# Performance work log

Measured on AMD Instinct MI355X. Metric: run time of the kernel, lower is better.

## Reference

```python
import jax, jax.numpy as jnp
import numpy as np

EPS = 1e-08


def _norm(H, add):
    # Faithful to GTN.norm: transpose, mask/set diagonal, row-normalize by degree, transpose back.
    # The original O(N^3) mm(deg_inv_diag, H) is expressed as an O(N^2) row scaling (same math).
    Ht = H.T
    n = Ht.shape[0]
    eye = jnp.eye(n, dtype=H.dtype)
    Ht = Ht * (1.0 - eye)
    if add:
        Ht = Ht + eye
    deg = jnp.sum(Ht, axis=1)
    deg_inv = jnp.where(deg == 0, 0.0, 1.0 / (deg + EPS))
    return (deg_inv[:, None] * Ht).T


def _gtconv(A, w):
    # A: [E, N, N]; w: [C, E, 1, 1] -> softmax over E, weighted sum of adjacency channels.
    s = jax.nn.softmax(w[:, :, 0, 0], axis=1)  # [C, E]
    return jnp.einsum('ce,eij->cij', s, A)     # [C, N, N]


def setup_inputs() -> dict:
    key = jax.random.key(0)
    k = jax.random.split(key, 6)
    E, N, C, w_in, w_out = 5, 2048, 2, 256, 64
    A = jax.random.uniform(k[0], (E, N, N), dtype=jnp.float32)
    X = jax.random.normal(k[1], (N, w_in), dtype=jnp.float32)
    conv_w_l0_1 = jax.random.normal(k[2], (C, E, 1, 1), dtype=jnp.float32)
    conv_w_l0_2 = jax.random.normal(k[3], (C, E, 1, 1), dtype=jnp.float32)
    conv_w_l1 = jax.random.normal(k[4], (C, E, 1, 1), dtype=jnp.float32)
    gcn_weight = jax.random.normal(k[5], (w_in, w_out), dtype=jnp.float32) * (1.0 / np.sqrt(w_in))
    return {"A": A, "X": X, "conv_w_l0_1": conv_w_l0_1, "conv_w_l0_2": conv_w_l0_2,
            "conv_w_l1": conv_w_l1, "gcn_weight": gcn_weight}


def reference(A, X, conv_w_l0_1, conv_w_l0_2, conv_w_l1, gcn_weight):
    N = A.shape[1]
    # Layer 0 (first=True): two GTConvs, meta-path composition via bmm.
    a = _gtconv(A, conv_w_l0_1)            # [C, N, N]
    b = _gtconv(A, conv_w_l0_2)            # [C, N, N]
    H = jnp.einsum('cij,cjk->cik', a, b)   # [C, N, N]
    # Layer 1 (first=False): normalize per channel, then compose with new conv.
    H = jax.vmap(lambda h: _norm(h, False))(H)
    a1 = _gtconv(A, conv_w_l1)
    H = jnp.einsum('cij,cjk->cik', H, a1)
    # GCN readout per channel: mm(norm_add(H_c).T, X @ W), relu, concat along features.
    Xw = X @ gcn_weight                     # [N, w_out]
    Hn = jax.vmap(lambda h: _norm(h, True))(H)   # [C, N, N]
    Xc = jax.nn.relu(jnp.einsum('cji,jk->cik', Hn, Xw))  # [C, N, w_out]
    X_ = jnp.transpose(Xc, (1, 0, 2)).reshape(N, -1)     # [N, C*w_out]
    return X_
```

## Files before the change

### kernel.cpp

```cpp
#include <hip/hip_runtime.h>
#include <cstdint>
#include <cstddef>

typedef unsigned short u16;
typedef __attribute__((ext_vector_type(8))) short short8;
typedef __attribute__((ext_vector_type(4))) float v4f;

static constexpr size_t NN = (size_t)2048 * 2048;
#define N2 2048

typedef __attribute__((address_space(1))) const unsigned int guint;
typedef __attribute__((address_space(3))) unsigned int luint;

__device__ __forceinline__ float b2f_bits(uint32_t hi) { union { uint32_t u; float f; } v; v.u = hi; return v.f; }
__device__ __forceinline__ float b2f(u16 x) { return b2f_bits((uint32_t)x << 16); }
__device__ __forceinline__ u16 f2b(float f) {
  union { float f; uint32_t u; } v; v.f = f;
  uint32_t r = v.u + 0x7fffu + ((v.u >> 16) & 1u);
  return (u16)(r >> 16);
}
__device__ __forceinline__ uint4 pack8(const float* f) {
  uint4 u;
  u.x = (uint32_t)f2b(f[0]) | ((uint32_t)f2b(f[1]) << 16);
  u.y = (uint32_t)f2b(f[2]) | ((uint32_t)f2b(f[3]) << 16);
  u.z = (uint32_t)f2b(f[4]) | ((uint32_t)f2b(f[5]) << 16);
  u.w = (uint32_t)f2b(f[6]) | ((uint32_t)f2b(f[7]) << 16);
  return u;
}
__device__ __forceinline__ float sgprf(float x) {
  union { float f; int i; } v; v.f = x;
  v.i = __builtin_amdgcn_readfirstlane(v.i);
  return v.f;
}

__global__ __launch_bounds__(512, 2) void conv_kernel(
    const float* __restrict__ A, const float* __restrict__ w1,
    const float* __restrict__ w2, const float* __restrict__ w3,
    const float* __restrict__ X, const float* __restrict__ W,
    u16* __restrict__ abf, u16* __restrict__ bbt, u16* __restrict__ a1t,
    u16* __restrict__ a1r, u16* __restrict__ Xwt, int* __restrict__ counters)
{
  __shared__ u16 LT[2][64 * 64];
  const int t = threadIdx.x;
  const int i0 = blockIdx.y * 64, j0 = blockIdx.x * 64;
  const int m = t >> 3;
  const int cg = t & 7;
  const int n0 = cg * 8;

  if (blockIdx.x == 0 && blockIdx.y == 0 && t < 66) counters[t] = 0;

  float sc[3][2][5];
  {
    const float* wsrc[3] = { w1, w2, w3 };
    for (int q = 0; q < 3; ++q)
      for (int c = 0; c < 2; ++c) {
        float v[5], mx = -1e30f, sum = 0.f;
        #pragma unroll
        for (int e = 0; e < 5; ++e) { v[e] = wsrc[q][c * 5 + e]; mx = fmaxf(mx, v[e]); }
        #pragma unroll
        for (int e = 0; e < 5; ++e) { v[e] = expf(v[e] - mx); sum += v[e]; }
        #pragma unroll
        for (int e = 0; e < 5; ++e) sc[q][c][e] = sgprf(v[e] / sum);
      }
  }

  float av[2][8], bv[2][8], cv[2][8];
  #pragma unroll
  for (int c = 0; c < 2; ++c)
    #pragma unroll
    for (int u = 0; u < 8; ++u) { av[c][u] = 0.f; bv[c][u] = 0.f; cv[c][u] = 0.f; }

  #pragma unroll
  for (int e = 0; e < 5; ++e) {
    const float* base = A + (size_t)e * NN + (size_t)(i0 + m) * N2 + (j0 + n0);
    float4 x0 = ((const float4*)base)[0];
    float4 x1 = ((const float4*)base)[1];
    float f[8] = { x0.x, x0.y, x0.z, x0.w, x1.x, x1.y, x1.z, x1.w };
    #pragma unroll
    for (int c = 0; c < 2; ++c)
      #pragma unroll
      for (int u = 0; u < 8; ++u) {
        av[c][u] += sc[0][c][e] * f[u];
        bv[c][u] += sc[1][c][e] * f[u];
        cv[c][u] += sc[2][c][e] * f[u];
      }
  }

  #pragma unroll
  for (int c = 0; c < 2; ++c) {
    *(uint4*)(abf + (size_t)c * NN + (size_t)(i0 + m) * N2 + (j0 + n0)) = pack8(av[c]);
    *(uint4*)(a1r + (size_t)c * NN + (size_t)(i0 + m) * N2 + (j0 + n0)) = pack8(cv[c]);
  }
  const int swb = ((m >> 3) ^ cg) & 7;
  const int mlo = m & 7;
  const int on = t >> 3;
  const int mb = t & 7;
  const int src = on * 64 + (((mb ^ (on >> 3)) & 7) * 8);
  #pragma unroll
  for (int c = 0; c < 2; ++c) {
    if (c == 1) __syncthreads();
    #pragma unroll
    for (int u = 0; u < 8; ++u) {
      const int idx = (n0 + u) * 64 + swb * 8 + mlo;
      LT[0][idx] = f2b(bv[c][u]);
      LT[1][idx] = f2b(cv[c][u]);
    }
    __syncthreads();
    *(uint4*)(bbt + (size_t)c * NN + (size_t)(j0 + on) * N2 + (i0 + mb * 8)) =
        *(const uint4*)&LT[0][src];
    *(uint4*)(a1t + (size_t)c * NN + (size_t)(j0 + on) * N2 + (i0 + mb * 8)) =
        *(const uint4*)&LT[1][src];
  }
  if (blockIdx.y < 8) {
    const int n = (int)(blockIdx.y * 32 + blockIdx.x) * 8 + (t >> 6);
    const int k = t & 63;
    float acc = 0.f;
    for (int mm = 0; mm < 256; ++mm)
      acc += X[n * 256 + mm] * W[mm * 64 + k];
    Xwt[(size_t)k * N2 + n] = f2b(acc);
  }
}

__global__ __launch_bounds__(256, 3) void gemm_kernel(
    const u16* __restrict__ Ain, const u16* __restrict__ Btin,
    u16* __restrict__ Cout, float* __restrict__ csp, float* __restrict__ diag)
{
  const int c = blockIdx.z;
  const u16* Ac = Ain + (size_t)c * NN;
  const u16* Bc = Btin + (size_t)c * NN;
  const int m0 = blockIdx.y * 128, n0 = blockIdx.x * 128;
  const int t = threadIdx.x, w = t >> 6, lane = t & 63;
  const int quad = lane >> 4, r = lane & 15;
  __shared__ u16 SM[128 * 64 + 128 * 64];
  u16* As = SM;
  u16* Bs = SM + 128 * 64;

  v4f zero4 = { 0.f, 0.f, 0.f, 0.f };
  v4f acc[2][8];
  #pragma unroll
  for (int i = 0; i < 2; ++i)
    #pragma unroll
    for (int j = 0; j < 8; ++j) acc[i][j] = zero4;

  const int srow = lane >> 3;
  const int sgran = (lane & 7) ^ srow;

  for (int kt = 0; kt < 2048; kt += 64) {
    __syncthreads();
    #pragma unroll
    for (int i = 0; i < 4; ++i) {
      const int chunk = i * 4 + w;
      const u16* ga = Ac + (size_t)(m0 + chunk * 8 + srow) * N2 + kt + sgran * 8;
      __builtin_amdgcn_global_load_lds((guint*)ga, (luint*)(As + chunk * 512), 16, 0, 0);
    }
    #pragma unroll
    for (int i = 0; i < 4; ++i) {
      const int chunk = i * 4 + w;
      const u16* gb = Bc + (size_t)(n0 + chunk * 8 + srow) * N2 + kt + sgran * 8;
      __builtin_amdgcn_global_load_lds((guint*)gb, (luint*)(Bs + chunk * 512), 16, 0, 0);
    }
    __syncthreads();
    #pragma unroll
    for (int ks = 0; ks < 2; ++ks) {
      const int sl = ((ks * 4 + quad) ^ (r & 7)) * 8;
      short8 af[2], bf[8];
      #pragma unroll
      for (int i = 0; i < 2; ++i)
        af[i] = *(const short8*)(As + (w * 32 + i * 16 + r) * 64 + sl);
      #pragma unroll
      for (int j = 0; j < 8; ++j)
        bf[j] = *(const short8*)(Bs + (j * 16 + r) * 64 + sl);
      #pragma unroll
      for (int i = 0; i < 2; ++i)
        #pragma unroll
        for (int j = 0; j < 8; ++j)
          acc[i][j] = __builtin_amdgcn_mfma_f32_16x16x32_bf16(af[i], bf[j], acc[i][j], 0, 0, 0);
    }
  }
  if (blockIdx.x == blockIdx.y) {
    #pragma unroll
    for (int i = 0; i < 2; ++i) {
      const int rowg = m0 + w * 32 + i * 16 + quad * 4;
      #pragma unroll
      for (int j = 0; j < 8; ++j) {
        const int colg = n0 + j * 16 + r;
        #pragma unroll
        for (int g = 0; g < 4; ++g)
          if (rowg + g == colg) diag[c * N2 + colg] = acc[i][j][g];
      }
    }
  }
  float s[8];
  #pragma unroll
  for (int j = 0; j < 8; ++j) {
    s[j] = 0.f;
    #pragma unroll
    for (int i = 0; i < 2; ++i)
      #pragma unroll
      for (int g = 0; g < 4; ++g) s[j] += acc[i][j][g];
    s[j] += __shfl_xor(s[j], 16);
    s[j] += __shfl_xor(s[j], 32);
  }
  __syncthreads();
  float* csl = (float*)SM;
  if (quad == 0) {
    #pragma unroll
    for (int j = 0; j < 8; ++j) csl[w * 128 + j * 16 + r] = s[j];
  }
  __syncthreads();
  if (t < 128) {
    const float v = csl[t] + csl[128 + t] + csl[256 + t] + csl[384 + t];
    csp[((size_t)(c * 16) + blockIdx.y) * N2 + n0 + t] = v;
  }
  {
    u16* tb = SM;
    u16* Cc = Cout + (size_t)c * NN;
    #pragma unroll
    for (int h = 0; h < 2; ++h) {
      __syncthreads();
      #pragma unroll
      for (int i = 0; i < 2; ++i) {
        #pragma unroll
        for (int jl = 0; jl < 4; ++jl) {
          const int j = h * 4 + jl;
          #pragma unroll
          for (int g = 0; g < 4; ++g)
            tb[(jl * 16 + r) * 136 + (w * 32 + i * 16 + quad * 4 + g)] = f2b(acc[i][j][g]);
        }
      }
      __syncthreads();
      const int rown = t >> 2, seg = t & 3;
      const u16* ps = tb + rown * 136 + seg * 32;
      uint4* pd = (uint4*)(Cc + (size_t)(n0 + h * 64 + rown) * N2 + m0 + seg * 32);
      pd[0] = ((const uint4*)ps)[0];
      pd[1] = ((const uint4*)ps)[1];
      pd[2] = ((const uint4*)ps)[2];
      pd[3] = ((const uint4*)ps)[3];
    }
  }
}

__global__ __launch_bounds__(256) void zgemm_kernel(
    const u16* __restrict__ Ht, const u16* __restrict__ Xwt,
    const u16* __restrict__ a1r, const float* __restrict__ csp,
    const float* __restrict__ diag1, float* __restrict__ Zp,
    float* __restrict__ dp, float* __restrict__ cp,
    u16* __restrict__ Yt, float* __restrict__ diag2, float* __restrict__ dinv2,
    int* __restrict__ counters)
{
  const int c = blockIdx.z, split = blockIdx.y, mt = blockIdx.x;
  const int m0 = mt * 128;
  const u16* Ac = Ht + (size_t)c * NN;
  const int t = threadIdx.x, w = t >> 6, lane = t & 63;
  const int quad = lane >> 4, r = lane & 15;
  __shared__ u16 SMZ[128 * 64 + 64 * 64];
  u16* As = SMZ;
  u16* Bs = SMZ + 128 * 64;

  v4f zero4 = { 0.f, 0.f, 0.f, 0.f };
  v4f acc[2][4];
  #pragma unroll
  for (int i = 0; i < 2; ++i)
    #pragma unroll
    for (int j = 0; j < 4; ++j) acc[i][j] = zero4;

  const int srow = lane >> 3;
  const int sgran = (lane & 7) ^ srow;

  for (int kk = 0; kk < 4; ++kk) {
    const int kt = split * 256 + kk * 64;
    __syncthreads();
    #pragma unroll
    for (int i = 0; i < 4; ++i) {
      const int chunk = i * 4 + w;
      const u16* ga = Ac + (size_t)(m0 + chunk * 8 + srow) * N2 + kt + sgran * 8;
      __builtin_amdgcn_global_load_lds((guint*)ga, (luint*)(As + chunk * 512), 16, 0, 0);
    }
    #pragma unroll
    for (int i = 0; i < 2; ++i) {
      const int chunk = i * 4 + w;
      const u16* gb = Xwt + (size_t)(chunk * 8 + srow) * N2 + kt + sgran * 8;
      __builtin_amdgcn_global_load_lds((guint*)gb, (luint*)(Bs + chunk * 512), 16, 0, 0);
    }
    __syncthreads();
    #pragma unroll
    for (int ks = 0; ks < 2; ++ks) {
      const int sl = ((ks * 4 + quad) ^ (r & 7)) * 8;
      short8 af[2], bf[4];
      #pragma unroll
      for (int i = 0; i < 2; ++i)
        af[i] = *(const short8*)(As + (w * 32 + i * 16 + r) * 64 + sl);
      #pragma unroll
      for (int j = 0; j < 4; ++j)
        bf[j] = *(const short8*)(Bs + (j * 16 + r) * 64 + sl);
      #pragma unroll
      for (int i = 0; i < 2; ++i)
        #pragma unroll
        for (int j = 0; j < 4; ++j)
          acc[i][j] = __builtin_amdgcn_mfma_f32_16x16x32_bf16(af[i], bf[j], acc[i][j], 0, 0, 0);
    }
  }
  const size_t pbase = (size_t)(split * 2 + c) * 64;
  #pragma unroll
  for (int i = 0; i < 2; ++i) {
    const int rowg = m0 + w * 32 + i * 16 + quad * 4;
    #pragma unroll
    for (int j = 0; j < 4; ++j) {
      const int colg = j * 16 + r;
      *(v4f*)(Zp + (pbase + colg) * (size_t)N2 + rowg) = acc[i][j];
    }
  }
  __syncthreads();
  float* ci_l = (float*)SMZ;
  float* wv_l = ci_l + 128;
  if (t < 128) {
    const int i = m0 + t;
    float cs = 0.f;
    #pragma unroll
    for (int s = 0; s < 16; ++s) cs += csp[((size_t)(c * 16) + s) * N2 + i];
    const float deg = cs - diag1[c * N2 + i];
    const float v = (deg == 0.f) ? 0.f : 1.f / (deg + 1e-8f);
    ci_l[t] = v;
    wv_l[t] = v * deg;
  }
  __syncthreads();
  const int j4 = (t & 15) * 4, ig = t >> 4;
  float dacc[4][4], cacc[4][4];
  #pragma unroll
  for (int kk = 0; kk < 4; ++kk) {
    const int gj = split * 256 + kk * 64 + j4;
    #pragma unroll
    for (int u = 0; u < 4; ++u) { dacc[kk][u] = 0.f; cacc[kk][u] = 0.f; }
    for (int ii = 0; ii < 8; ++ii) {
      const int i = m0 + ig * 8 + ii;
      uint2 hu = *(const uint2*)(Ht  + (size_t)c * NN + (size_t)i * N2 + gj);
      uint2 au = *(const uint2*)(a1r + (size_t)c * NN + (size_t)i * N2 + gj);
      float h[4], a[4];
      h[0] = b2f_bits(hu.x << 16); h[1] = b2f_bits(hu.x & 0xffff0000u);
      h[2] = b2f_bits(hu.y << 16); h[3] = b2f_bits(hu.y & 0xffff0000u);
      a[0] = b2f_bits(au.x << 16); a[1] = b2f_bits(au.x & 0xffff0000u);
      a[2] = b2f_bits(au.y << 16); a[3] = b2f_bits(au.y & 0xffff0000u);
      const float cq = ci_l[ig * 8 + ii];
      const float wq = wv_l[ig * 8 + ii];
      #pragma unroll
      for (int u = 0; u < 4; ++u) {
        cacc[kk][u] += wq * a[u];
        const float tv = cq * h[u] * a[u];
        dacc[kk][u] += (i == gj + u) ? 0.f : tv;
      }
    }
  }
  float* red = ci_l + 256;
  __syncthreads();
  #pragma unroll
  for (int kk = 0; kk < 4; ++kk)
    #pragma unroll
    for (int u = 0; u < 4; ++u) red[ig * 256 + kk * 64 + j4 + u] = dacc[kk][u];
  __syncthreads();
  {
    float v = 0.f;
    #pragma unroll
    for (int g = 0; g < 16; ++g) v += red[g * 256 + t];
    dp[((size_t)(c * 16) + mt) * N2 + split * 256 + t] = v;
  }
  __syncthreads();
  #pragma unroll
  for (int kk = 0; kk < 4; ++kk)
    #pragma unroll
    for (int u = 0; u < 4; ++u) red[ig * 256 + kk * 64 + j4 + u] = cacc[kk][u];
  __syncthreads();
  {
    float v = 0.f;
    #pragma unroll
    for (int g = 0; g < 16; ++g) v += red[g * 256 + t];
    cp[((size_t)(c * 16) + mt) * N2 + split * 256 + t] = v;
  }
  __shared__ int yLast, fLast;
  __syncthreads();
  if (t == 0) {
    __threadfence();
    yLast = (atomicAdd(&counters[mt * 2 + c], 1) == 7);
    fLast = (atomicAdd(&counters[32 + c], 1) == 127);
  }
  __syncthreads();
  if (yLast) {
    __threadfence();
    const int i = m0 + (t & 127), kg = t >> 7;
    const float civ = ci_l[t & 127];
    const float d1 = diag1[c * N2 + i];
    for (int k2 = 0; k2 < 32; ++k2) {
      const int k = kg * 32 + k2;
      float z = 0.f;
      #pragma unroll
      for (int s = 0; s < 8; ++s)
        z += Zp[(size_t)((s * 2 + c) * 64 + k) * N2 + i];
      const float xw = b2f(Xwt[(size_t)k * N2 + i]);
      Yt[(size_t)(c * 64 + k) * N2 + i] = f2b(civ * (z - d1 * xw));
    }
  }
  if (fLast) {
    __threadfence();
    for (int q = t; q < 2048; q += 256) {
      float ds = 0.f, cs = 0.f;
      #pragma unroll
      for (int b = 0; b < 16; ++b) {
        ds += dp[((size_t)(c * 16) + b) * N2 + q];
        cs += cp[((size_t)(c * 16) + b) * N2 + q];
      }
      const float deg = cs - ds + 1.0f;
      diag2[c * N2 + q] = ds;
      dinv2[c * N2 + q] = (deg == 0.f) ? 0.f : 1.f / (deg + 1e-8f);
    }
  }
}

__global__ __launch_bounds__(256) void tgemm_kernel(
    const u16* __restrict__ a1t, const u16* __restrict__ Yt,
    float* __restrict__ Tp, const float* __restrict__ diag2,
    const float* __restrict__ dinv2, const u16* __restrict__ Xwt,
    float* __restrict__ out, int* __restrict__ counters)
{
  const int c = blockIdx.z, split = blockIdx.y, mt = blockIdx.x;
  const int m0 = mt * 128;
  const u16* Ac = a1t + (size_t)c * NN;
  const u16* Bc = Yt + (size_t)c * (64 * (size_t)N2);
  const int t = threadIdx.x, w = t >> 6, lane = t & 63;
  const int quad = lane >> 4, r = lane & 15;
  __shared__ u16 As[128 * 64];
  __shared__ u16 Bs[64 * 64];

  v4f zero4 = { 0.f, 0.f, 0.f, 0.f };
  v4f acc[2][4];
  #pragma unroll
  for (int i = 0; i < 2; ++i)
    #pragma unroll
    for (int j = 0; j < 4; ++j) acc[i][j] = zero4;

  const int srow = lane >> 3;
  const int sgran = (lane & 7) ^ srow;

  for (int kk = 0; kk < 4; ++kk) {
    const int kt = split * 256 + kk * 64;
    __syncthreads();
    #pragma unroll
    for (int i = 0; i < 4; ++i) {
      const int chunk = i * 4 + w;
      const u16* ga = Ac + (size_t)(m0 + chunk * 8 + srow) * N2 + kt + sgran * 8;
      __builtin_amdgcn_global_load_lds((guint*)ga, (luint*)(As + chunk * 512), 16, 0, 0);
    }
    #pragma unroll
    for (int i = 0; i < 2; ++i) {
      const int chunk = i * 4 + w;
      const u16* gb = Bc + (size_t)(chunk * 8 + srow) * N2 + kt + sgran * 8;
      __builtin_amdgcn_global_load_lds((guint*)gb, (luint*)(Bs + chunk * 512), 16, 0, 0);
    }
    __syncthreads();
    #pragma unroll
    for (int ks = 0; ks < 2; ++ks) {
      const int sl = ((ks * 4 + quad) ^ (r & 7)) * 8;
      short8 af[2], bf[4];
      #pragma unroll
      for (int i = 0; i < 2; ++i)
        af[i] = *(const short8*)(As + (w * 32 + i * 16 + r) * 64 + sl);
      #pragma unroll
      for (int j = 0; j < 4; ++j)
        bf[j] = *(const short8*)(Bs + (j * 16 + r) * 64 + sl);
      #pragma unroll
      for (int i = 0; i < 2; ++i)
        #pragma unroll
        for (int j = 0; j < 4; ++j)
          acc[i][j] = __builtin_amdgcn_mfma_f32_16x16x32_bf16(af[i], bf[j], acc[i][j], 0, 0, 0);
    }
  }
  const size_t pbase = (size_t)(split * 2 + c) * 2048;
  #pragma unroll
  for (int i = 0; i < 2; ++i) {
    const int rowg = m0 + w * 32 + i * 16 + quad * 4;
    #pragma unroll
    for (int j = 0; j < 4; ++j) {
      const int colg = j * 16 + r;
      #pragma unroll
      for (int g = 0; g < 4; ++g)
        Tp[(pbase + rowg + g) * 64 + colg] = acc[i][j][g];
    }
  }
  __shared__ int eLast;
  __syncthreads();
  if (t == 0) {
    __threadfence();
    eLast = (atomicAdd(&counters[34 + mt * 2 + c], 1) == 7);
  }
  __syncthreads();
  if (eLast) {
    __threadfence();
    const int k = t & 63, ig = t >> 6;
    for (int ii = 0; ii < 32; ++ii) {
      const int i = m0 + ig * 32 + ii;
      float T = 0.f;
      #pragma unroll
      for (int s = 0; s < 8; ++s)
        T += Tp[((size_t)(s * 2 + c) * 2048 + i) * 64 + k];
      const float hd = diag2[c * N2 + i];
      const float dv = dinv2[c * N2 + i];
      const float xw = b2f(Xwt[(size_t)k * N2 + i]);
      float v = dv * (T - hd * xw + xw);
      v = v > 0.f ? v : 0.f;
      out[(size_t)i * 128 + c * 64 + k] = v;
    }
  }
}

extern "C" void kernel_launch(void* const* d_in, const int* in_sizes, int n_in,
                              void* d_out, int out_size, void* d_ws, size_t ws_size,
                              hipStream_t stream) {
  const float* A  = (const float*)d_in[0];
  const float* X  = (const float*)d_in[1];
  const float* w1 = (const float*)d_in[2];
  const float* w2 = (const float*)d_in[3];
  const float* w3 = (const float*)d_in[4];
  const float* W  = (const float*)d_in[5];
  float* out = (float*)d_out;
  char* ws = (char*)d_ws;

  u16*   abf   = (u16*)(ws + 0);
  u16*   bbt   = (u16*)(ws + 16777216);
  u16*   a1t   = (u16*)(ws + 33554432);
  u16*   a1r   = (u16*)(ws + 50331648);
  u16*   Ht    = (u16*)(ws + 67108864);
  u16*   Xwt   = (u16*)(ws + 83886080);
  float* cspa  = (float*)(ws + 84148224);
  float* diag1 = (float*)(ws + 84410368);
  float* diag2 = (float*)(ws + 84426752);
  float* dinv2 = (float*)(ws + 84443136);
  int*   cnt   = (int*)  (ws + 84459520);
  float* Zp    = (float*)(ws + 0);
  float* dp    = (float*)(ws + 16777216);
  float* cp    = (float*)(ws + 17039360);
  u16*   Yt    = (u16*)(ws + 17301504);
  float* Tp    = (float*)(ws + 50331648);

  conv_kernel<<<dim3(32, 32), 512, 0, stream>>>(A, w1, w2, w3, X, W, abf, bbt, a1t, a1r, Xwt, cnt);
  gemm_kernel<<<dim3(16, 16, 2), 256, 0, stream>>>(abf, bbt, Ht, cspa, diag1);
  zgemm_kernel<<<dim3(16, 8, 2), 256, 0, stream>>>(Ht, Xwt, a1r, cspa, diag1, Zp, dp, cp, Yt, diag2, dinv2, cnt);
  tgemm_kernel<<<dim3(16, 8, 2), 256, 0, stream>>>(a1t, Yt, Tp, diag2, dinv2, Xwt, out, cnt);
}
```

Baseline: 258.6 us.

## Replace split-K partial buffers with atomic accumulation and fuse Y construction into tgemm

Both skinny GEMMs now accumulate their split-K results straight into zeroed Z and T buffers with float atomics, instead of writing per-split partials that a last-arriving block reduces. The Y = D^-1(Z - diag*Xw) operand is no longer materialized by zgemm's tail. Each tgemm block computes its 256-row slice of Y into LDS from Z, and the degree/diag2 reduction moves into tgemm's epilogue. Conv_kernel zeroes Z/T and spreads the Xw computation across all blocks. This removes serialized last-block tails and partial-buffer traffic, at the cost of atomic contention and redundant Y recomputation across the 16 m-tiles.

After: 262.3 us. No clear change (+1.4%).

```diff
diff --git a/kernel.cpp b/kernel.cpp
--- a/kernel.cpp
+++ b/kernel.cpp
@@ -38,16 +38,19 @@
     const float* __restrict__ w2, const float* __restrict__ w3,
     const float* __restrict__ X, const float* __restrict__ W,
     u16* __restrict__ abf, u16* __restrict__ bbt, u16* __restrict__ a1t,
-    u16* __restrict__ a1r, u16* __restrict__ Xwt, int* __restrict__ counters)
+    u16* __restrict__ a1r, u16* __restrict__ Xwt,
+    float* __restrict__ zeroZT, int* __restrict__ counters)
 {
   __shared__ u16 LT[2][64 * 64];
   const int t = threadIdx.x;
+  const int bid = (int)(blockIdx.y * 32 + blockIdx.x);
   const int i0 = blockIdx.y * 64, j0 = blockIdx.x * 64;
   const int m = t >> 3;
   const int cg = t & 7;
   const int n0 = cg * 8;
 
-  if (blockIdx.x == 0 && blockIdx.y == 0 && t < 66) counters[t] = 0;
+  zeroZT[(size_t)bid * 512 + t] = 0.f;
+  if (bid == 0 && t < 64) counters[t] = 0;
 
   float sc[3][2][5];
   {
@@ -111,8 +114,8 @@
     *(uint4*)(a1t + (size_t)c * NN + (size_t)(j0 + on) * N2 + (i0 + mb * 8)) =
         *(const uint4*)&LT[1][src];
   }
-  if (blockIdx.y < 8) {
-    const int n = (int)(blockIdx.y * 32 + blockIdx.x) * 8 + (t >> 6);
+  if (t < 128) {
+    const int n = bid * 2 + (t >> 6);
     const int k = t & 63;
     float acc = 0.f;
     for (int mm = 0; mm < 256; ++mm)
@@ -243,10 +246,8 @@
 __global__ __launch_bounds__(256) void zgemm_kernel(
     const u16* __restrict__ Ht, const u16* __restrict__ Xwt,
     const u16* __restrict__ a1r, const float* __restrict__ csp,
-    const float* __restrict__ diag1, float* __restrict__ Zp,
-    float* __restrict__ dp, float* __restrict__ cp,
-    u16* __restrict__ Yt, float* __restrict__ diag2, float* __restrict__ dinv2,
-    int* __restrict__ counters)
+    const float* __restrict__ diag1, float* __restrict__ Z,
+    float* __restrict__ dp, float* __restrict__ cp)
 {
   const int c = blockIdx.z, split = blockIdx.y, mt = blockIdx.x;
   const int m0 = mt * 128;
@@ -300,14 +301,16 @@
           acc[i][j] = __builtin_amdgcn_mfma_f32_16x16x32_bf16(af[i], bf[j], acc[i][j], 0, 0, 0);
     }
   }
-  const size_t pbase = (size_t)(split * 2 + c) * 64;
   #pragma unroll
   for (int i = 0; i < 2; ++i) {
     const int rowg = m0 + w * 32 + i * 16 + quad * 4;
     #pragma unroll
     for (int j = 0; j < 4; ++j) {
       const int colg = j * 16 + r;
-      *(v4f*)(Zp + (pbase + colg) * (size_t)N2 + rowg) = acc[i][j];
+      float* base = Z + (size_t)(c * 64 + colg) * N2 + rowg;
+      #pragma unroll
+      for (int g = 0; g < 4; ++g)
+        atomicAdd(base + g, acc[i][j][g]);
     }
   }
   __syncthreads();
@@ -375,59 +378,45 @@
     for (int g = 0; g < 16; ++g) v += red[g * 256 + t];
     cp[((size_t)(c * 16) + mt) * N2 + split * 256 + t] = v;
   }
-  __shared__ int yLast, fLast;
-  __syncthreads();
-  if (t == 0) {
-    __threadfence();
-    yLast = (atomicAdd(&counters[mt * 2 + c], 1) == 7);
-    fLast = (atomicAdd(&counters[32 + c], 1) == 127);
-  }
-  __syncthreads();
-  if (yLast) {
-    __threadfence();
-    const int i = m0 + (t & 127), kg = t >> 7;
-    const float civ = ci_l[t & 127];
-    const float d1 = diag1[c * N2 + i];
-    for (int k2 = 0; k2 < 32; ++k2) {
-      const int k = kg * 32 + k2;
-      float z = 0.f;
-      #pragma unroll
-      for (int s = 0; s < 8; ++s)
-        z += Zp[(size_t)((s * 2 + c) * 64 + k) * N2 + i];
-      const float xw = b2f(Xwt[(size_t)k * N2 + i]);
-      Yt[(size_t)(c * 64 + k) * N2 + i] = f2b(civ * (z - d1 * xw));
-    }
-  }
-  if (fLast) {
-    __threadfence();
-    for (int q = t; q < 2048; q += 256) {
-      float ds = 0.f, cs = 0.f;
-      #pragma unroll
-      for (int b = 0; b < 16; ++b) {
-        ds += dp[((size_t)(c * 16) + b) * N2 + q];
-        cs += cp[((size_t)(c * 16) + b) * N2 + q];
-      }
-      const float deg = cs - ds + 1.0f;
-      diag2[c * N2 + q] = ds;
-      dinv2[c * N2 + q] = (deg == 0.f) ? 0.f : 1.f / (deg + 1e-8f);
-    }
-  }
 }
 
 __global__ __launch_bounds__(256) void tgemm_kernel(
-    const u16* __restrict__ a1t, const u16* __restrict__ Yt,
-    float* __restrict__ Tp, const float* __restrict__ diag2,
-    const float* __restrict__ dinv2, const u16* __restrict__ Xwt,
+    const u16* __restrict__ a1t, const float* __restrict__ csp,
+    const float* __restrict__ diag1, const float* __restrict__ Z,
+    const u16* __restrict__ Xwt, const float* __restrict__ dp,
+    const float* __restrict__ cp, float* __restrict__ T,
     float* __restrict__ out, int* __restrict__ counters)
 {
   const int c = blockIdx.z, split = blockIdx.y, mt = blockIdx.x;
-  const int m0 = mt * 128;
-  const u16* Ac = a1t + (size_t)c * NN;
-  const u16* Bc = Yt + (size_t)c * (64 * (size_t)N2);
+  const int m0 = mt * 128, kt0 = split * 256;
   const int t = threadIdx.x, w = t >> 6, lane = t & 63;
   const int quad = lane >> 4, r = lane & 15;
   __shared__ u16 As[128 * 64];
-  __shared__ u16 Bs[64 * 64];
+  __shared__ u16 Bp[64 * 256];
+  __shared__ float cif[256], d1f[256];
+
+  {
+    const int jj = kt0 + t;
+    float cs = 0.f;
+    #pragma unroll
+    for (int s = 0; s < 16; ++s) cs += csp[((size_t)(c * 16) + s) * N2 + jj];
+    const float d1 = diag1[c * N2 + jj];
+    const float deg = cs - d1;
+    cif[t] = (deg == 0.f) ? 0.f : 1.f / (deg + 1e-8f);
+    d1f[t] = d1;
+  }
+  __syncthreads();
+  {
+    const int kk = t >> 6, g = (t >> 3) & 7, el = t & 7;
+    const float civ = cif[t], d1v = d1f[t];
+    const float* zcol = Z + (size_t)(c * 64) * N2 + kt0 + t;
+    const u16* xcol = Xwt + kt0 + t;
+    for (int k = 0; k < 64; ++k) {
+      const float z = zcol[(size_t)k * N2];
+      const float xw = b2f(xcol[(size_t)k * N2]);
+      Bp[k * 256 + kk * 64 + ((g ^ (k & 7)) * 8) + el] = f2b(civ * (z - d1v * xw));
+    }
+  }
 
   v4f zero4 = { 0.f, 0.f, 0.f, 0.f };
   v4f acc[2][4];
@@ -440,19 +429,13 @@
   const int sgran = (lane & 7) ^ srow;
 
   for (int kk = 0; kk < 4; ++kk) {
-    const int kt = split * 256 + kk * 64;
+    const int kt = kt0 + kk * 64;
     __syncthreads();
     #pragma unroll
     for (int i = 0; i < 4; ++i) {
       const int chunk = i * 4 + w;
-      const u16* ga = Ac + (size_t)(m0 + chunk * 8 + srow) * N2 + kt + sgran * 8;
+      const u16* ga = a1t + (size_t)c * NN + (size_t)(m0 + chunk * 8 + srow) * N2 + kt + sgran * 8;
       __builtin_amdgcn_global_load_lds((guint*)ga, (luint*)(As + chunk * 512), 16, 0, 0);
-    }
-    #pragma unroll
-    for (int i = 0; i < 2; ++i) {
-      const int chunk = i * 4 + w;
-      const u16* gb = Bc + (size_t)(chunk * 8 + srow) * N2 + kt + sgran * 8;
-      __builtin_amdgcn_global_load_lds((guint*)gb, (luint*)(Bs + chunk * 512), 16, 0, 0);
     }
     __syncthreads();
     #pragma unroll
@@ -464,7 +447,7 @@
         af[i] = *(const short8*)(As + (w * 32 + i * 16 + r) * 64 + sl);
       #pragma unroll
       for (int j = 0; j < 4; ++j)
-        bf[j] = *(const short8*)(Bs + (j * 16 + r) * 64 + sl);
+        bf[j] = *(const short8*)(Bp + (j * 16 + r) * 256 + kk * 64 + sl);
       #pragma unroll
       for (int i = 0; i < 2; ++i)
         #pragma unroll
@@ -472,38 +455,42 @@
           acc[i][j] = __builtin_amdgcn_mfma_f32_16x16x32_bf16(af[i], bf[j], acc[i][j], 0, 0, 0);
     }
   }
-  const size_t pbase = (size_t)(split * 2 + c) * 2048;
   #pragma unroll
   for (int i = 0; i < 2; ++i) {
     const int rowg = m0 + w * 32 + i * 16 + quad * 4;
     #pragma unroll
     for (int j = 0; j < 4; ++j) {
       const int colg = j * 16 + r;
+      float* base = T + ((size_t)(c * 2048) + rowg) * 64 + colg;
       #pragma unroll
       for (int g = 0; g < 4; ++g)
-        Tp[(pbase + rowg + g) * 64 + colg] = acc[i][j][g];
+        atomicAdd(base + (size_t)g * 64, acc[i][j][g]);
     }
   }
   __shared__ int eLast;
   __syncthreads();
   if (t == 0) {
     __threadfence();
-    eLast = (atomicAdd(&counters[34 + mt * 2 + c], 1) == 7);
+    eLast = (atomicAdd(&counters[mt * 2 + c], 1) == 7);
   }
   __syncthreads();
   if (eLast) {
     __threadfence();
-    const int k = t & 63, ig = t >> 6;
-    for (int ii = 0; ii < 32; ++ii) {
-      const int i = m0 + ig * 32 + ii;
-      float T = 0.f;
-      #pragma unroll
-      for (int s = 0; s < 8; ++s)
-        T += Tp[((size_t)(s * 2 + c) * 2048 + i) * 64 + k];
-      const float hd = diag2[c * N2 + i];
-      const float dv = dinv2[c * N2 + i];
+    const int i = m0 + (t >> 1), kh = (t & 1) * 32;
+    float ds = 0.f, cs = 0.f;
+    #pragma unroll
+    for (int b = 0; b < 16; ++b) {
+      ds += dp[((size_t)(c * 16) + b) * N2 + i];
+      cs += cp[((size_t)(c * 16) + b) * N2 + i];
+    }
+    const float deg = cs - ds + 1.0f;
+    const float dv = (deg == 0.f) ? 0.f : 1.f / (deg + 1e-8f);
+    #pragma unroll
+    for (int k2 = 0; k2 < 32; ++k2) {
+      const int k = kh + k2;
+      const float Tv = T[((size_t)(c * 2048) + i) * 64 + k];
       const float xw = b2f(Xwt[(size_t)k * N2 + i]);
-      float v = dv * (T - hd * xw + xw);
+      float v = dv * (Tv - ds * xw + xw);
       v = v > 0.f ? v : 0.f;
       out[(size_t)i * 128 + c * 64 + k] = v;
     }
@@ -530,17 +517,14 @@
   u16*   Xwt   = (u16*)(ws + 83886080);
   float* cspa  = (float*)(ws + 84148224);
   float* diag1 = (float*)(ws + 84410368);
-  float* diag2 = (float*)(ws + 84426752);
-  float* dinv2 = (float*)(ws + 84443136);
-  int*   cnt   = (int*)  (ws + 84459520);
-  float* Zp    = (float*)(ws + 0);
-  float* dp    = (float*)(ws + 16777216);
-  float* cp    = (float*)(ws + 17039360);
-  u16*   Yt    = (u16*)(ws + 17301504);
-  float* Tp    = (float*)(ws + 50331648);
-
-  conv_kernel<<<dim3(32, 32), 512, 0, stream>>>(A, w1, w2, w3, X, W, abf, bbt, a1t, a1r, Xwt, cnt);
+  float* dp    = (float*)(ws + 84426752);
+  float* cp    = (float*)(ws + 84688896);
+  float* Z     = (float*)(ws + 84951040);
+  float* T     = (float*)(ws + 85999616);
+  int*   cnt   = (int*)  (ws + 87048192);
+
+  conv_kernel<<<dim3(32, 32), 512, 0, stream>>>(A, w1, w2, w3, X, W, abf, bbt, a1t, a1r, Xwt, Z, cnt);
   gemm_kernel<<<dim3(16, 16, 2), 256, 0, stream>>>(abf, bbt, Ht, cspa, diag1);
-  zgemm_kernel<<<dim3(16, 8, 2), 256, 0, stream>>>(Ht, Xwt, a1r, cspa, diag1, Zp, dp, cp, Yt, diag2, dinv2, cnt);
-  tgemm_kernel<<<dim3(16, 8, 2), 256, 0, stream>>>(a1t, Yt, Tp, diag2, dinv2, Xwt, out, cnt);
-}
+  zgemm_kernel<<<dim3(16, 8, 2), 256, 0, stream>>>(Ht, Xwt, a1r, cspa, diag1, Z, dp, cp);
+  tgemm_kernel<<<dim3(16, 8, 2), 256, 0, stream>>>(a1t, cspa, diag1, Z, Xwt, dp, cp, T, out, cnt);
+}
```
